# Kernel optimization log

Hardware: AMD Instinct MI355X
Metric: run time of the kernel (lower is better)

Reference implementation:

```python
import jax, jax.numpy as jnp
import numpy as np

N = 5000
NFEAT = 512
NHID = 64
NHEADS = 8
NCLASS = 40
ALPHA = 0.2  # leaky relu slope
NEG_INF = -9e15


def setup_inputs() -> dict:
    key = jax.random.key(0)
    ks = jax.random.split(key, 12)
    x = jax.random.normal(ks[0], (N, NFEAT), dtype=jnp.float32)
    # binary adjacency, ~32 avg degree, with self loops
    adj = (jax.random.uniform(ks[1], (N, N)) < (32.0 / N)).astype(jnp.float32)
    adj = jnp.maximum(adj, jnp.eye(N, dtype=jnp.float32))
    s = 1.0 / np.sqrt(NFEAT)
    W_h = jax.random.uniform(ks[2], (NHEADS, NFEAT, NHID), minval=-s, maxval=s, dtype=jnp.float32)
    a_h = jax.random.uniform(ks[3], (NHEADS, 2 * NHID), minval=-s, maxval=s, dtype=jnp.float32)
    s2 = 1.0 / np.sqrt(NHID * NHEADS)
    W_o = jax.random.uniform(ks[4], (NHID * NHEADS, NHID), minval=-s2, maxval=s2, dtype=jnp.float32)
    a_o = jax.random.uniform(ks[5], (2 * NHID,), minval=-s2, maxval=s2, dtype=jnp.float32)
    s3 = 1.0 / np.sqrt(NHID)
    fc1_w = jax.random.uniform(ks[6], (NHID, 200), minval=-s3, maxval=s3, dtype=jnp.float32)
    fc1_b = jax.random.uniform(ks[7], (200,), minval=-s3, maxval=s3, dtype=jnp.float32)
    s4 = 1.0 / np.sqrt(200)
    fc2_w = jax.random.uniform(ks[8], (200, NCLASS), minval=-s4, maxval=s4, dtype=jnp.float32)
    fc2_b = jax.random.uniform(ks[9], (NCLASS,), minval=-s4, maxval=s4, dtype=jnp.float32)
    return {"x": x, "adj": adj, "W_h": W_h, "a_h": a_h, "W_o": W_o, "a_o": a_o,
            "fc1_w": fc1_w, "fc1_b": fc1_b, "fc2_w": fc2_w, "fc2_b": fc2_b}


def _masked_attention(e, adj):
    # e: [..., N, N]; mask where adj == 0, then row softmax
    e = jnp.where(adj > 0, e, NEG_INF)
    return jax.nn.softmax(e, axis=-1)


def reference(x, adj, W_h, a_h, W_o, a_o, fc1_w, fc1_b, fc2_w, fc2_b):
    # ---- multi-head GAT layer (concat=True), eval mode (dropout off) ----
    Wh = jnp.einsum('nf,hfo->hno', x, W_h)                 # [H, N, nhid]
    f1 = jnp.einsum('hno,ho->hn', Wh, a_h[:, :NHID])       # [H, N]
    f2 = jnp.einsum('hno,ho->hn', Wh, a_h[:, NHID:])       # [H, N]
    e = jax.nn.leaky_relu(f1[:, :, None] + f2[:, None, :], ALPHA)  # [H, N, N]
    att = _masked_attention(e, adj[None, :, :])
    h = jnp.einsum('hnm,hmo->hno', att, Wh)                # [H, N, nhid]
    h1 = jax.nn.elu(h).transpose(1, 0, 2).reshape(N, NHEADS * NHID)  # concat heads

    # ---- output GAT layer (concat=False) ----
    Wh2 = h1 @ W_o                                         # [N, nhid]
    g1 = Wh2 @ a_o[:NHID]                                  # [N]
    g2 = Wh2 @ a_o[NHID:]                                  # [N]
    e2 = jax.nn.leaky_relu(g1[:, None] + g2[None, :], ALPHA)
    att2 = _masked_attention(e2, adj)
    h2 = att2 @ Wh2                                        # [N, nhid]

    # ---- MLP head ----
    h3 = jax.nn.elu(h2 @ fc1_w + fc1_b)
    return h3 @ fc2_w + fc2_b                              # [N, nclass]
```

## Files before the change

### kernel.cpp

```cpp
#include <hip/hip_runtime.h>

typedef unsigned short u16;
typedef unsigned int u32;
typedef unsigned long long u64;
typedef __bf16 bf16_t;
typedef __bf16 bf16x8 __attribute__((ext_vector_type(8)));
typedef u16 u16x8 __attribute__((ext_vector_type(8)));
typedef float f32x4 __attribute__((ext_vector_type(4)));
typedef u32 u32x4 __attribute__((ext_vector_type(4)));

#define NN 5000
#define NF 512
#define NH 64
#define HEADS 8
#define NCLS 40
#define CAP 128
#define LRELU 0.2f

#define G1_BLKS (79 * HEADS)
#define ADJ_BLKS 2500
#define K1_GRID (G1_BLKS + ADJ_BLKS)
#define W0_BLKS 64
#define PRM_BLKS 8
#define K0_GRID (W0_BLKS + PRM_BLKS)

__device__ __forceinline__ bool adj_is_bf16(const void* adj) {
    return ((*(const u32*)adj) & 0xFFFFu) != 0u;
}
__device__ __forceinline__ u16 rne_bf16(float f) {
    u32 u = __float_as_uint(f);
    u += 0x7FFFu + ((u >> 16) & 1u);
    return (u16)(u >> 16);
}
__device__ __forceinline__ float up_bf16(u16 h) {
    return __uint_as_float((u32)h << 16);
}
__device__ __forceinline__ float in_f32(const void* p, int idx, bool isb) {
    return isb ? up_bf16(((const u16*)p)[idx]) : ((const float*)p)[idx];
}
__device__ __forceinline__ u32x4 ntload4(const void* p, int idx) {
    return __builtin_nontemporal_load(((const u32x4*)p) + idx);
}
union U8cast { u16x8 u; bf16x8 b; };

__global__ __launch_bounds__(256) void cvt_w(const void* __restrict__ W_h,
                                             const void* __restrict__ adj,
                                             const void* W_o, const void* a_o,
                                             const void* f1w, const void* f1b,
                                             const void* f2w, const void* f2b,
                                             u16* __restrict__ whc,
                                             float* W_oc, float* a_oc,
                                             float* f1wc, float* f1bc,
                                             float* f2wc, float* f2bc) {
    const bool isb = adj_is_bf16(adj);
    const int b = blockIdx.x;
    if (b < W0_BLKS) {
        const int W4 = HEADS * NF * NH / 4;
        for (int iw = b * 256 + threadIdx.x; iw < W4; iw += W0_BLKS * 256) {
            u16 q[4];
            if (isb) {
                ushort4 vv = ((const ushort4*)W_h)[iw];
                q[0] = vv.x; q[1] = vv.y; q[2] = vv.z; q[3] = vv.w;
            } else {
                u32x4 vv = ntload4(W_h, iw);
                q[0] = rne_bf16(__uint_as_float(vv[0])); q[1] = rne_bf16(__uint_as_float(vv[1]));
                q[2] = rne_bf16(__uint_as_float(vv[2])); q[3] = rne_bf16(__uint_as_float(vv[3]));
            }
            const int e0 = iw * 4;
            const int h = e0 >> 15;
            const int rem = e0 & 32767;
            const int f = rem >> 6, o0 = rem & 63;
            const int base = (h * 16 + (f >> 5)) * 2048 + ((f >> 3) & 3) * 128 + (f & 7);
            #pragma unroll
            for (int k = 0; k < 4; ++k) {
                const int o = o0 + k;
                whc[base + (o >> 4) * 512 + (o & 15) * 8] = q[k];
            }
        }
    } else {
        const int s1 = HEADS * NH * NH, s2 = 2 * NH,
                  s3 = NH * 200, s4 = 200, s5 = 200 * NCLS, s6 = NCLS;
        const int total = s1 + s2 + s3 + s4 + s5 + s6;
        const int pb = b - W0_BLKS;
        for (int i = pb * 256 + threadIdx.x; i < total; i += PRM_BLKS * 256) {
            const void* src; float* dst; int off = i;
            if (off < s1) { src = W_o;  dst = W_oc; }
            else if ((off -= s1) < s2) { src = a_o;  dst = a_oc; }
            else if ((off -= s2) < s3) { src = f1w;  dst = f1wc; }
            else if ((off -= s3) < s4) { src = f1b;  dst = f1bc; }
            else if ((off -= s4) < s5) { src = f2w;  dst = f2wc; }
            else { off -= s5;           src = f2b;  dst = f2bc; }
            dst[off] = isb ? up_bf16(((const u16*)src)[off]) : ((const float*)src)[off];
        }
    }
}

__global__ __launch_bounds__(256) void gemm1_f(const void* __restrict__ x,
                                               const bf16_t* __restrict__ Wf,
                                               const void* __restrict__ a_h,
                                               const void* __restrict__ adj,
                                               int* __restrict__ nbr, int* __restrict__ deg,
                                               float* __restrict__ Wh,
                                               float* __restrict__ f1,
                                               float* __restrict__ f2) {
    const int lane = threadIdx.x & 63;
    const int wid  = threadIdx.x >> 6;
    const int b = blockIdx.x;
    __shared__ float f1s[4][64], f2s[4][64];
    __shared__ int s_cnt[4];

    if (b >= G1_BLKS) {
        const bool isb = adj_is_bf16(adj);
        const int a = b - G1_BLKS;
        const int r = a * 2 + (wid >> 1);
        const int hf = wid & 1;
        u64 myw = 0ull;
        if (!isb) {
            const float* row = (const float*)adj + (size_t)r * NN;
            u32x4 v[10];
            #pragma unroll
            for (int k = 0; k < 10; ++k) {
                int c = hf * 640 + k * 64 + lane;
                v[k] = (c < 1250) ? ntload4(row, c) : (u32x4){0u, 0u, 0u, 0u};
            }
            #pragma unroll
            for (int k = 0; k < 10; ++k) {
                #pragma unroll
                for (int j = 0; j < 4; ++j) {
                    u64 m = __ballot(v[k][j] != 0u);
                    if (k * 4 + j == lane) myw = m;
                }
            }
        } else {
            const u16* row = (const u16*)adj + (size_t)r * NN;
            u32x4 v[5];
            #pragma unroll
            for (int k = 0; k < 5; ++k) {
                int c = hf * 320 + k * 64 + lane;
                v[k] = (c < 625) ? ntload4(row, c) : (u32x4){0u, 0u, 0u, 0u};
            }
            #pragma unroll
            for (int k = 0; k < 5; ++k) {
                #pragma unroll
                for (int j = 0; j < 4; ++j) {
                    u64 mlo = __ballot((v[k][j] & 0xFFFFu) != 0u);
                    u64 mhi = __ballot((v[k][j] >> 16) != 0u);
                    int wl = k * 8 + 2 * j;
                    if (wl == lane)     myw = mlo;
                    if (wl + 1 == lane) myw = mhi;
                }
            }
        }
        int pc = __popcll(myw);
        int scan = pc;
        #pragma unroll
        for (int o = 1; o < 64; o <<= 1) {
            int t2 = __shfl_up(scan, o);
            if (lane >= o) scan += t2;
        }
        const int cnt = __shfl(scan, 63);
        if (lane == 0) s_cnt[wid] = cnt;
        __syncthreads();
        const int base0 = hf ? s_cnt[wid - 1] : 0;
        int off = base0 + scan - pc;
        int* nrow = nbr + (size_t)r * CAP;
        const int w = hf * 40 + lane;
        u64 mw = myw;
        while (mw) {
            int bb = __ffsll(mw) - 1;
            mw &= mw - 1;
            int elem = !isb ? ((w >> 2) * 64 + bb) * 4 + (w & 3)
                            : ((w >> 3) * 64 + bb) * 8 + (w & 7);
            if (off < CAP) nrow[off] = elem;
            ++off;
        }
        if (hf == 1 && lane == 0) {
            int tot = base0 + cnt;
            deg[r] = tot < CAP ? tot : CAP;
        }
        return;
    }

    const bool isb = adj_is_bf16(adj);
    const int rg = b % 79;
    const int h  = b / 79;
    const int quad = lane >> 4;
    const int lr   = lane & 15;
    const int kq   = quad * 8;
    const int nCol = wid * 16 + lr;

    const bf16_t* Bf = Wf + (size_t)h * (16 * 2048) + threadIdx.x * 8;
    bf16x8 bfrag[16];
    #pragma unroll
    for (int s = 0; s < 16; ++s) bfrag[s] = *(const bf16x8*)(Bf + s * 2048);

    const float a1c = in_f32(a_h, h * 128 + nCol, isb);
    const float a2c = in_f32(a_h, h * 128 + NH + nCol, isb);

    for (int t = 0; t < 4; ++t) {
        const int rb = rg * 64 + t * 16;
        int row  = rb + lr;
        int rowc = row < NN ? row : NN - 1;
        f32x4 acc = {0.f, 0.f, 0.f, 0.f};
        if (!isb) {
            const float* xp = (const float*)x + (size_t)rowc * NF + kq;
            #pragma unroll
            for (int s = 0; s < 16; ++s) {
                float4 lo = *(const float4*)(xp + s * 32);
                float4 hi = *(const float4*)(xp + s * 32 + 4);
                bf16x8 a;
                a[0] = (bf16_t)lo.x; a[1] = (bf16_t)lo.y; a[2] = (bf16_t)lo.z; a[3] = (bf16_t)lo.w;
                a[4] = (bf16_t)hi.x; a[5] = (bf16_t)hi.y; a[6] = (bf16_t)hi.z; a[7] = (bf16_t)hi.w;
                acc = __builtin_amdgcn_mfma_f32_16x16x32_bf16(a, bfrag[s], acc, 0, 0, 0);
            }
        } else {
            const u16* xp = (const u16*)x + (size_t)rowc * NF + kq;
            #pragma unroll
            for (int s = 0; s < 16; ++s) {
                U8cast cc;
                cc.u = *(const u16x8*)(xp + s * 32);
                acc = __builtin_amdgcn_mfma_f32_16x16x32_bf16(cc.b, bfrag[s], acc, 0, 0, 0);
            }
        }
        #pragma unroll
        for (int r = 0; r < 4; ++r) {
            int gr = rb + quad * 4 + r;
            if (gr < NN) Wh[(size_t)gr * (HEADS * NH) + h * NH + nCol] = acc[r];
            float p1 = acc[r] * a1c, p2 = acc[r] * a2c;
            #pragma unroll
            for (int o = 8; o; o >>= 1) { p1 += __shfl_xor(p1, o); p2 += __shfl_xor(p2, o); }
            if (lr == 0) { f1s[wid][t * 16 + quad * 4 + r] = p1; f2s[wid][t * 16 + quad * 4 + r] = p2; }
        }
    }
    __syncthreads();
    if (wid == 0) {
        int gr = rg * 64 + lane;
        if (gr < NN) {
            f1[h * NN + gr] = f1s[0][lane] + f1s[1][lane] + f1s[2][lane] + f1s[3][lane];
            f2[h * NN + gr] = f2s[0][lane] + f2s[1][lane] + f2s[2][lane] + f2s[3][lane];
        }
    }
}

__global__ __launch_bounds__(256) void agg1f(const int* __restrict__ nbr,
                                             const int* __restrict__ deg,
                                             const float* __restrict__ Wh,
                                             const float* __restrict__ f1,
                                             const float* __restrict__ f2,
                                             float* __restrict__ h1) {
    const int lane = threadIdx.x & 63;
    const int wid  = threadIdx.x >> 6;
    const int n = blockIdx.x;
    __shared__ int s_nbr[CAP];
    __shared__ float s_p[8][CAP];
    const int d = deg[n];
    for (int i = threadIdx.x; i < d; i += 256) s_nbr[i] = nbr[(size_t)n * CAP + i];
    __syncthreads();

    const int ha = wid, hb = wid + 4;
    const int nb0 = (lane < d) ? s_nbr[lane] : 0;
    const int nb1 = (lane + 64 < d) ? s_nbr[lane + 64] : 0;
    const float f10 = f1[ha * NN + n], f11 = f1[hb * NN + n];
    const float* f2ha = f2 + (size_t)ha * NN;
    const float* f2hb = f2 + (size_t)hb * NN;

    float e00 = -INFINITY, e01 = -INFINITY, e10 = -INFINITY, e11 = -INFINITY;
    if (lane < d) {
        float a = f10 + f2ha[nb0]; e00 = a > 0.f ? a : LRELU * a;
        float b = f11 + f2hb[nb0]; e10 = b > 0.f ? b : LRELU * b;
    }
    if (lane + 64 < d) {
        float a = f10 + f2ha[nb1]; e01 = a > 0.f ? a : LRELU * a;
        float b = f11 + f2hb[nb1]; e11 = b > 0.f ? b : LRELU * b;
    }
    float mx0 = fmaxf(e00, e01), mx1 = fmaxf(e10, e11);
    #pragma unroll
    for (int o = 32; o; o >>= 1) {
        mx0 = fmaxf(mx0, __shfl_xor(mx0, o));
        mx1 = fmaxf(mx1, __shfl_xor(mx1, o));
    }
    float p00 = lane < d ? expf(e00 - mx0) : 0.f;
    float p01 = lane + 64 < d ? expf(e01 - mx0) : 0.f;
    float p10 = lane < d ? expf(e10 - mx1) : 0.f;
    float p11 = lane + 64 < d ? expf(e11 - mx1) : 0.f;
    float sm0 = p00 + p01, sm1 = p10 + p11;
    #pragma unroll
    for (int o = 32; o; o >>= 1) { sm0 += __shfl_xor(sm0, o); sm1 += __shfl_xor(sm1, o); }

    const float i0 = 1.f / sm0, i1 = 1.f / sm1;
    s_p[ha][lane] = p00 * i0; s_p[ha][lane + 64] = p01 * i0;
    s_p[hb][lane] = p10 * i1; s_p[hb][lane + 64] = p11 * i1;
    __syncthreads();

    const float* ap = s_p[2 * wid + (lane >> 5)];
    const float* wp = Wh + wid * 128 + 2 * lane;
    float A0x = 0.f, A0y = 0.f, A1x = 0.f, A1y = 0.f;
    float A2x = 0.f, A2y = 0.f, A3x = 0.f, A3y = 0.f;
    int j = 0;
    for (; j + 8 <= d; j += 8) {
        #pragma unroll
        for (int u = 0; u < 8; ++u) {
            const float2 v = *(const float2*)(wp + (size_t)s_nbr[j + u] * (HEADS * NH));
            const float a = ap[j + u];
            if ((u & 3) == 0)      { A0x += a * v.x; A0y += a * v.y; }
            else if ((u & 3) == 1) { A1x += a * v.x; A1y += a * v.y; }
            else if ((u & 3) == 2) { A2x += a * v.x; A2y += a * v.y; }
            else                   { A3x += a * v.x; A3y += a * v.y; }
        }
    }
    for (; j < d; ++j) {
        const float2 v = *(const float2*)(wp + (size_t)s_nbr[j] * (HEADS * NH));
        const float a = ap[j];
        A0x += a * v.x; A0y += a * v.y;
    }
    float hx = A0x + A1x + A2x + A3x;
    float hy = A0y + A1y + A2y + A3y;
    hx = hx > 0.f ? hx : expf(hx) - 1.f;
    hy = hy > 0.f ? hy : expf(hy) - 1.f;
    *(float2*)(h1 + (size_t)n * (HEADS * NH) + wid * 128 + 2 * lane) = make_float2(hx, hy);
}

__global__ __launch_bounds__(256) void gemm2_4(const float* __restrict__ h1,
                                               const float* __restrict__ W_o,
                                               const float* __restrict__ a_o,
                                               float* __restrict__ Wh2,
                                               float* __restrict__ g1,
                                               float* __restrict__ g2) {
    const int t = threadIdx.x;
    const int n0 = blockIdx.x * 4;
    __shared__ float sh[4 * 512];
    __shared__ float ps[4][4][64];
    const float4* src = (const float4*)(h1 + (size_t)n0 * 512);
    ((float4*)sh)[t]       = src[t];
    ((float4*)sh)[t + 256] = src[t + 256];
    __syncthreads();
    const int o = t & 63, part = t >> 6;
    float a0 = 0.f, a1 = 0.f, a2 = 0.f, a3 = 0.f;
    const float* wo = W_o + part * 128 * 64 + o;
    const float* s0 = sh + part * 128;
    #pragma unroll 4
    for (int f = 0; f < 128; ++f) {
        float w = wo[f * 64];
        a0 += s0[f] * w; a1 += s0[512 + f] * w; a2 += s0[1024 + f] * w; a3 += s0[1536 + f] * w;
    }
    ps[part][0][o] = a0; ps[part][1][o] = a1; ps[part][2][o] = a2; ps[part][3][o] = a3;
    __syncthreads();
    const int nd = t >> 6;
    float w2 = ps[0][nd][o] + ps[1][nd][o] + ps[2][nd][o] + ps[3][nd][o];
    Wh2[(size_t)(n0 + nd) * 64 + o] = w2;
    float p1 = w2 * a_o[o], p2 = w2 * a_o[64 + o];
    #pragma unroll
    for (int s = 32; s; s >>= 1) { p1 += __shfl_xor(p1, s); p2 += __shfl_xor(p2, s); }
    if (o == 0) { g1[n0 + nd] = p1; g2[n0 + nd] = p2; }
}

__global__ __launch_bounds__(256) void agg2_mlp(const float* __restrict__ Wh2,
                                                const float* __restrict__ g1,
                                                const float* __restrict__ g2,
                                                const int* __restrict__ nbr,
                                                const int* __restrict__ deg,
                                                const float* __restrict__ fc1_w,
                                                const float* __restrict__ fc1_b,
                                                const float* __restrict__ fc2_w,
                                                const float* __restrict__ fc2_b,
                                                float* __restrict__ out) {
    const int lane = threadIdx.x & 63;
    const int wid  = threadIdx.x >> 6;
    const int t = threadIdx.x;
    const int n0 = blockIdx.x * 4;
    const int n = n0 + wid;
    __shared__ float s_alpha[4][CAP];
    __shared__ int   s_nbr[4][CAP];
    __shared__ float s_h2[4][NH];
    __shared__ float s_h3[4][200];
    __shared__ float ps2[2][4][NCLS];
    const int d = deg[n];
    const int* nb = nbr + (size_t)n * CAP;
    const float gn = g1[n];

    float mx = -INFINITY;
    for (int j = lane; j < d; j += 64) {
        int m = nb[j];
        s_nbr[wid][j] = m;
        float e = gn + g2[m];
        e = e > 0.f ? e : LRELU * e;
        s_alpha[wid][j] = e;
        mx = fmaxf(mx, e);
    }
    #pragma unroll
    for (int o = 32; o; o >>= 1) mx = fmaxf(mx, __shfl_xor(mx, o));
    float sm = 0.f;
    for (int j = lane; j < d; j += 64) {
        float p = expf(s_alpha[wid][j] - mx);
        s_alpha[wid][j] = p;
        sm += p;
    }
    #pragma unroll
    for (int o = 32; o; o >>= 1) sm += __shfl_xor(sm, o);

    float acc0 = 0.f, acc1 = 0.f, acc2 = 0.f, acc3 = 0.f;
    int j = 0;
    for (; j + 4 <= d; j += 4) {
        acc0 += s_alpha[wid][j]     * Wh2[(size_t)s_nbr[wid][j]     * NH + lane];
        acc1 += s_alpha[wid][j + 1] * Wh2[(size_t)s_nbr[wid][j + 1] * NH + lane];
        acc2 += s_alpha[wid][j + 2] * Wh2[(size_t)s_nbr[wid][j + 2] * NH + lane];
        acc3 += s_alpha[wid][j + 3] * Wh2[(size_t)s_nbr[wid][j + 3] * NH + lane];
    }
    for (; j < d; ++j) acc0 += s_alpha[wid][j] * Wh2[(size_t)s_nbr[wid][j] * NH + lane];
    s_h2[wid][lane] = (acc0 + acc1 + acc2 + acc3) / sm;
    __syncthreads();

    if (t < 200) {
        float b0 = 0.f, b1 = 0.f, b2 = 0.f, b3 = 0.f;
        #pragma unroll 4
        for (int f = 0; f < NH; ++f) {
            float w = fc1_w[f * 200 + t];
            b0 += s_h2[0][f] * w; b1 += s_h2[1][f] * w; b2 += s_h2[2][f] * w; b3 += s_h2[3][f] * w;
        }
        float bb = fc1_b[t];
        b0 += bb; b1 += bb; b2 += bb; b3 += bb;
        s_h3[0][t] = b0 > 0.f ? b0 : expf(b0) - 1.f;
        s_h3[1][t] = b1 > 0.f ? b1 : expf(b1) - 1.f;
        s_h3[2][t] = b2 > 0.f ? b2 : expf(b2) - 1.f;
        s_h3[3][t] = b3 > 0.f ? b3 : expf(b3) - 1.f;
    }
    __syncthreads();

    if (t < 80) {
        const int o = t % 40, fh = t / 40;
        float c0 = 0.f, c1 = 0.f, c2 = 0.f, c3 = 0.f;
        #pragma unroll 4
        for (int f = fh * 100; f < fh * 100 + 100; ++f) {
            float w = fc2_w[f * NCLS + o];
            c0 += s_h3[0][f] * w; c1 += s_h3[1][f] * w; c2 += s_h3[2][f] * w; c3 += s_h3[3][f] * w;
        }
        ps2[fh][0][o] = c0; ps2[fh][1][o] = c1; ps2[fh][2][o] = c2; ps2[fh][3][o] = c3;
    }
    __syncthreads();
    if (t < 160) {
        const int nd = t / 40, o = t % 40;
        out[(size_t)(n0 + nd) * NCLS + o] = ps2[0][nd][o] + ps2[1][nd][o] + fc2_b[o];
    }
}

extern "C" void kernel_launch(void* const* d_in, const int* in_sizes, int n_in,
                              void* d_out, int out_size, void* d_ws, size_t ws_size,
                              hipStream_t stream) {
    const void* x     = d_in[0];
    const void* adj   = d_in[1];
    const void* W_h   = d_in[2];
    const void* a_h   = d_in[3];
    const void* W_o   = d_in[4];
    const void* a_o   = d_in[5];
    const void* fc1_w = d_in[6];
    const void* fc1_b = d_in[7];
    const void* fc2_w = d_in[8];
    const void* fc2_b = d_in[9];
    float* out = (float*)d_out;

    char* ws = (char*)d_ws;
    int*   nbr   = (int*)(ws + 0);
    int*   deg   = (int*)(ws + 2560000);
    float* Wh    = (float*)(ws + 2580000);
    float* f1    = (float*)(ws + 12820000);
    float* f2    = (float*)(ws + 12980000);
    float* h1    = (float*)(ws + 13140000);
    float* Wh2   = (float*)(ws + 23380000);
    float* g1    = (float*)(ws + 24660000);
    float* g2    = (float*)(ws + 24680000);
    float* W_oc  = (float*)(ws + 24700000);
    float* a_oc  = (float*)(ws + 24831072);
    float* f1wc  = (float*)(ws + 24831584);
    float* f1bc  = (float*)(ws + 24882784);
    float* f2wc  = (float*)(ws + 24883584);
    float* f2bc  = (float*)(ws + 24915584);
    u16*   whc   = (u16*)(ws + 24915744);

    cvt_w<<<K0_GRID, 256, 0, stream>>>(W_h, adj, W_o, a_o, fc1_w, fc1_b, fc2_w, fc2_b,
                                       whc, W_oc, a_oc, f1wc, f1bc, f2wc, f2bc);
    gemm1_f<<<K1_GRID, 256, 0, stream>>>(x, (const bf16_t*)whc, a_h, adj,
                                         nbr, deg, Wh, f1, f2);
    agg1f<<<NN, 256, 0, stream>>>(nbr, deg, Wh, f1, f2, h1);
    gemm2_4<<<NN / 4, 256, 0, stream>>>(h1, W_oc, a_oc, Wh2, g1, g2);
    agg2_mlp<<<NN / 4, 256, 0, stream>>>(Wh2, g1, g2, nbr, deg,
                                         f1wc, f1bc, f2wc, f2bc, out);
}
```

Measured before the change: 282.7 us.

## Move adjacency compaction from GEMM kernel into first-layer aggregation kernel

The dense adjacency scan that builds neighbor lists moves out of the extra blocks of the first GEMM kernel and into the start of the per-node aggregation kernel. Each block now compacts its own row into shared memory, so aggregation no longer has to read nbr/deg back from global memory, and the GEMM launch shrinks to just the compute blocks. In exchange, the 100MB adjacency stream now runs inside the aggregation kernel rather than alongside the GEMM, which loses that overlap. It also lengthens the aggregation kernel's critical path with a block-wide sync and scan.

```diff
diff --git a/kernel.cpp b/kernel.cpp
--- a/kernel.cpp
+++ b/kernel.cpp
@@ -18,8 +18,6 @@
 #define LRELU 0.2f
 
 #define G1_BLKS (79 * HEADS)
-#define ADJ_BLKS 2500
-#define K1_GRID (G1_BLKS + ADJ_BLKS)
 #define W0_BLKS 64
 #define PRM_BLKS 8
 #define K0_GRID (W0_BLKS + PRM_BLKS)
@@ -95,99 +93,23 @@
     }
 }
 
-__global__ __launch_bounds__(256) void gemm1_f(const void* __restrict__ x,
-                                               const bf16_t* __restrict__ Wf,
-                                               const void* __restrict__ a_h,
-                                               const void* __restrict__ adj,
-                                               int* __restrict__ nbr, int* __restrict__ deg,
-                                               float* __restrict__ Wh,
-                                               float* __restrict__ f1,
-                                               float* __restrict__ f2) {
+__global__ __launch_bounds__(256) void gemm1(const void* __restrict__ x,
+                                             const bf16_t* __restrict__ Wf,
+                                             const void* __restrict__ a_h,
+                                             const void* __restrict__ adj,
+                                             float* __restrict__ Wh,
+                                             float* __restrict__ f1,
+                                             float* __restrict__ f2) {
+    const bool isb = adj_is_bf16(adj);
     const int lane = threadIdx.x & 63;
     const int wid  = threadIdx.x >> 6;
-    const int b = blockIdx.x;
-    __shared__ float f1s[4][64], f2s[4][64];
-    __shared__ int s_cnt[4];
-
-    if (b >= G1_BLKS) {
-        const bool isb = adj_is_bf16(adj);
-        const int a = b - G1_BLKS;
-        const int r = a * 2 + (wid >> 1);
-        const int hf = wid & 1;
-        u64 myw = 0ull;
-        if (!isb) {
-            const float* row = (const float*)adj + (size_t)r * NN;
-            u32x4 v[10];
-            #pragma unroll
-            for (int k = 0; k < 10; ++k) {
-                int c = hf * 640 + k * 64 + lane;
-                v[k] = (c < 1250) ? ntload4(row, c) : (u32x4){0u, 0u, 0u, 0u};
-            }
-            #pragma unroll
-            for (int k = 0; k < 10; ++k) {
-                #pragma unroll
-                for (int j = 0; j < 4; ++j) {
-                    u64 m = __ballot(v[k][j] != 0u);
-                    if (k * 4 + j == lane) myw = m;
-                }
-            }
-        } else {
-            const u16* row = (const u16*)adj + (size_t)r * NN;
-            u32x4 v[5];
-            #pragma unroll
-            for (int k = 0; k < 5; ++k) {
-                int c = hf * 320 + k * 64 + lane;
-                v[k] = (c < 625) ? ntload4(row, c) : (u32x4){0u, 0u, 0u, 0u};
-            }
-            #pragma unroll
-            for (int k = 0; k < 5; ++k) {
-                #pragma unroll
-                for (int j = 0; j < 4; ++j) {
-                    u64 mlo = __ballot((v[k][j] & 0xFFFFu) != 0u);
-                    u64 mhi = __ballot((v[k][j] >> 16) != 0u);
-                    int wl = k * 8 + 2 * j;
-                    if (wl == lane)     myw = mlo;
-                    if (wl + 1 == lane) myw = mhi;
-                }
-            }
-        }
-        int pc = __popcll(myw);
-        int scan = pc;
-        #pragma unroll
-        for (int o = 1; o < 64; o <<= 1) {
-            int t2 = __shfl_up(scan, o);
-            if (lane >= o) scan += t2;
-        }
-        const int cnt = __shfl(scan, 63);
-        if (lane == 0) s_cnt[wid] = cnt;
-        __syncthreads();
-        const int base0 = hf ? s_cnt[wid - 1] : 0;
-        int off = base0 + scan - pc;
-        int* nrow = nbr + (size_t)r * CAP;
-        const int w = hf * 40 + lane;
-        u64 mw = myw;
-        while (mw) {
-            int bb = __ffsll(mw) - 1;
-            mw &= mw - 1;
-            int elem = !isb ? ((w >> 2) * 64 + bb) * 4 + (w & 3)
-                            : ((w >> 3) * 64 + bb) * 8 + (w & 7);
-            if (off < CAP) nrow[off] = elem;
-            ++off;
-        }
-        if (hf == 1 && lane == 0) {
-            int tot = base0 + cnt;
-            deg[r] = tot < CAP ? tot : CAP;
-        }
-        return;
-    }
-
-    const bool isb = adj_is_bf16(adj);
-    const int rg = b % 79;
-    const int h  = b / 79;
+    const int rg = blockIdx.x % 79;
+    const int h  = blockIdx.x / 79;
     const int quad = lane >> 4;
     const int lr   = lane & 15;
     const int kq   = quad * 8;
     const int nCol = wid * 16 + lr;
+    __shared__ float f1s[4][64], f2s[4][64];
 
     const bf16_t* Bf = Wf + (size_t)h * (16 * 2048) + threadIdx.x * 8;
     bf16x8 bfrag[16];
@@ -242,19 +164,85 @@
     }
 }
 
-__global__ __launch_bounds__(256) void agg1f(const int* __restrict__ nbr,
-                                             const int* __restrict__ deg,
-                                             const float* __restrict__ Wh,
-                                             const float* __restrict__ f1,
-                                             const float* __restrict__ f2,
-                                             float* __restrict__ h1) {
+__global__ __launch_bounds__(256) void adj_agg1(const void* __restrict__ adj,
+                                                const float* __restrict__ Wh,
+                                                const float* __restrict__ f1,
+                                                const float* __restrict__ f2,
+                                                int* __restrict__ nbr, int* __restrict__ deg,
+                                                float* __restrict__ h1) {
+    const bool isb = adj_is_bf16(adj);
     const int lane = threadIdx.x & 63;
     const int wid  = threadIdx.x >> 6;
     const int n = blockIdx.x;
     __shared__ int s_nbr[CAP];
     __shared__ float s_p[8][CAP];
-    const int d = deg[n];
-    for (int i = threadIdx.x; i < d; i += 256) s_nbr[i] = nbr[(size_t)n * CAP + i];
+    __shared__ int s_cnt[4];
+
+    u64 myw = 0ull;
+    if (!isb) {
+        const float* row = (const float*)adj + (size_t)n * NN;
+        u32x4 v[5];
+        #pragma unroll
+        for (int k = 0; k < 5; ++k) {
+            int c = (wid * 5 + k) * 64 + lane;
+            v[k] = (c < 1250) ? ntload4(row, c) : (u32x4){0u, 0u, 0u, 0u};
+        }
+        #pragma unroll
+        for (int k = 0; k < 5; ++k) {
+            #pragma unroll
+            for (int j = 0; j < 4; ++j) {
+                u64 m = __ballot(v[k][j] != 0u);
+                if (k * 4 + j == lane) myw = m;
+            }
+        }
+    } else {
+        const u16* row = (const u16*)adj + (size_t)n * NN;
+        u32x4 v[3];
+        #pragma unroll
+        for (int k = 0; k < 3; ++k) {
+            int kg = wid * 3 + k;
+            int c = kg * 64 + lane;
+            v[k] = (kg < 10 && c < 625) ? ntload4(row, c) : (u32x4){0u, 0u, 0u, 0u};
+        }
+        #pragma unroll
+        for (int k = 0; k < 3; ++k) {
+            #pragma unroll
+            for (int j = 0; j < 4; ++j) {
+                u64 mlo = __ballot((v[k][j] & 0xFFFFu) != 0u);
+                u64 mhi = __ballot((v[k][j] >> 16) != 0u);
+                int lw = k * 8 + 2 * j;
+                if (lw == lane)     myw = mlo;
+                if (lw + 1 == lane) myw = mhi;
+            }
+        }
+    }
+    int pc = __popcll(myw);
+    int scan = pc;
+    #pragma unroll
+    for (int o = 1; o < 64; o <<= 1) {
+        int t2 = __shfl_up(scan, o);
+        if (lane >= o) scan += t2;
+    }
+    if (lane == 63) s_cnt[wid] = scan;
+    __syncthreads();
+    int base = 0;
+    #pragma unroll
+    for (int wv = 0; wv < 3; ++wv) if (wv < wid) base += s_cnt[wv];
+    const int total = s_cnt[0] + s_cnt[1] + s_cnt[2] + s_cnt[3];
+    const int d = total < CAP ? total : CAP;
+    if (threadIdx.x == 0) deg[n] = d;
+    int off = base + scan - pc;
+    int* nrow = nbr + (size_t)n * CAP;
+    const int w = (isb ? wid * 24 : wid * 20) + lane;
+    u64 mw = myw;
+    while (mw) {
+        int bb = __ffsll(mw) - 1;
+        mw &= mw - 1;
+        int elem = !isb ? ((w >> 2) * 64 + bb) * 4 + (w & 3)
+                        : ((w >> 3) * 64 + bb) * 8 + (w & 7);
+        if (off < CAP) { s_nbr[off] = elem; nrow[off] = elem; }
+        ++off;
+    }
     __syncthreads();
 
     const int ha = wid, hb = wid + 4;
@@ -478,9 +466,8 @@
 
     cvt_w<<<K0_GRID, 256, 0, stream>>>(W_h, adj, W_o, a_o, fc1_w, fc1_b, fc2_w, fc2_b,
                                        whc, W_oc, a_oc, f1wc, f1bc, f2wc, f2bc);
-    gemm1_f<<<K1_GRID, 256, 0, stream>>>(x, (const bf16_t*)whc, a_h, adj,
-                                         nbr, deg, Wh, f1, f2);
-    agg1f<<<NN, 256, 0, stream>>>(nbr, deg, Wh, f1, f2, h1);
+    gemm1<<<G1_BLKS, 256, 0, stream>>>(x, (const bf16_t*)whc, a_h, adj, Wh, f1, f2);
+    adj_agg1<<<NN, 256, 0, stream>>>(adj, Wh, f1, f2, nbr, deg, h1);
     gemm2_4<<<NN / 4, 256, 0, stream>>>(h1, W_oc, a_oc, Wh2, g1, g2);
     agg2_mlp<<<NN / 4, 256, 0, stream>>>(Wh2, g1, g2, nbr, deg,
                                          f1wc, f1bc, f2wc, f2bc, out);
```

Result: no change. 285.4 us (+1.0%).
